# Optimization experiments

Measured on AMD Instinct MI355X. Metric: run time of the kernel, lower is better.

## Reference

```python
import jax, jax.numpy as jnp
import numpy as np
import math

N = 50000        # nodes
E = 800000       # edges
FEATS = 64
CLASSES = 16
HIDDEN = 64
DEPTH = 10
DIFF = 0.9
EMB_DIM = 1 + int(math.log2(FEATS))   # 7
ADJ_HID = 4 + EMB_DIM                  # 11


def setup_inputs() -> dict:
    key = jax.random.key(0)
    ks = jax.random.split(key, 12)
    x = jax.random.normal(ks[0], (N, FEATS), dtype=jnp.float32)
    src = jax.random.randint(ks[1], (E,), 0, N, dtype=jnp.int64)
    dst = jax.random.randint(ks[2], (E,), 0, N, dtype=jnp.int64)
    s = 0.05
    W1 = jax.random.normal(ks[3], (2 * FEATS, HIDDEN), jnp.float32) * s
    b1 = jnp.zeros((HIDDEN,), jnp.float32)
    W2 = jax.random.normal(ks[4], (HIDDEN, CLASSES), jnp.float32) * s
    b2 = jnp.zeros((CLASSES,), jnp.float32)
    A1 = jax.random.normal(ks[5], (2 + EMB_DIM, ADJ_HID), jnp.float32) * s
    ab1 = jnp.zeros((ADJ_HID,), jnp.float32)
    A2 = jax.random.normal(ks[6], (ADJ_HID, 1), jnp.float32) * s
    ab2 = jnp.zeros((1,), jnp.float32)
    emb = jax.random.normal(ks[7], (FEATS, EMB_DIM), jnp.float32) * s
    return {"x": x, "src": src, "dst": dst, "W1": W1, "b1": b1,
            "W2": W2, "b2": b2, "A1": A1, "ab1": ab1, "A2": A2,
            "ab2": ab2, "emb": emb}


def reference(x, src, dst, W1, b1, W2, b2, A1, ab1, A2, ab2, emb):
    n, f = x.shape
    # cached symmetric GCN normalization: D^-1/2 A D^-1/2
    deg = jax.ops.segment_sum(jnp.ones((src.shape[0],), x.dtype), dst, num_segments=n)
    inv_sqrt = jnp.where(deg > 0, jax.lax.rsqrt(jnp.maximum(deg, 1e-12)), 0.0)
    norm = inv_sqrt[src] * inv_sqrt[dst]   # [E]

    def conv(z):
        return jax.ops.segment_sum(z[src] * norm[:, None], dst, num_segments=n)

    # first diffusion loop (personalized-pagerank style residual blend)
    h0 = x
    z = x
    for _ in range(DEPTH):
        z = conv(z) * DIFF + (1.0 - DIFF) * h0

    # node x class pair MLP (class-major flatten, matching x.t().reshape(-1,1))
    cls = jnp.repeat(jnp.arange(f), n)                 # [f*n]
    pairs = jnp.concatenate([z.T.reshape(-1, 1),
                             h0.T.reshape(-1, 1),
                             emb[cls]], axis=1)        # [f*n, 2+EMB_DIM]
    u = jax.nn.relu(pairs @ A1 + ab1)
    u = (u @ A2 + ab2) / 2.0                           # [f*n, 1]
    z = u.reshape(f, n).T                              # [n, f]

    # dropout is identity in eval mode
    z = jnp.concatenate([z, h0], axis=1)               # [n, 2f]
    z = jax.nn.relu(z @ W1 + b1)
    z = z @ W2 + b2                                    # [n, classes]

    # second diffusion loop over class logits
    g0 = z
    for _ in range(DEPTH):
        z = conv(z) * DIFF + (1.0 - DIFF) * g0
    return z
```

## Files before the change

kernel.cpp:

```cpp
#include <hip/hip_runtime.h>

#define FEATS    64
#define CLASSES  16
#define EMB_DIM  7
#define ADJ_HID  11
#define DIFF     0.9f

__device__ inline float bf2f(unsigned short u) {
    return __uint_as_float(((unsigned int)u) << 16);
}
__device__ inline unsigned short f2bf(float f) {
    unsigned int u = __float_as_uint(f);
    return (unsigned short)((u + 0x7FFFu + ((u >> 16) & 1u)) >> 16);
}


__global__ __launch_bounds__(256) void k_deg(const int* __restrict__ dst, int* __restrict__ deg, int e) {
    int i = blockIdx.x * 256 + threadIdx.x;
    if (i < e) atomicAdd(&deg[dst[i]], 1);
}

__global__ __launch_bounds__(256) void k_invs(const int* __restrict__ deg, float* __restrict__ invs, int n) {
    int i = blockIdx.x * 256 + threadIdx.x;
    if (i < n) { int d = deg[i]; invs[i] = d > 0 ? rsqrtf((float)d) : 0.f; }
}

__global__ __launch_bounds__(256) void k_scan1(const int* __restrict__ deg, int* __restrict__ rowptr,
                                               int* __restrict__ bsum, int n) {
    __shared__ int s[256];
    int tid = threadIdx.x;
    int i = blockIdx.x * 256 + tid;
    int v = (i < n) ? deg[i] : 0;
    s[tid] = v; __syncthreads();
    for (int ofs = 1; ofs < 256; ofs <<= 1) {
        int t = (tid >= ofs) ? s[tid - ofs] : 0;
        __syncthreads(); s[tid] += t; __syncthreads();
    }
    if (i < n) rowptr[i] = s[tid] - v;
    if (tid == 255) bsum[blockIdx.x] = s[255];
}

__global__ __launch_bounds__(256) void k_scan2(int* __restrict__ bsum, int nb) {
    __shared__ int s[256];
    int tid = threadIdx.x;
    int v = (tid < nb) ? bsum[tid] : 0;
    s[tid] = v; __syncthreads();
    for (int ofs = 1; ofs < 256; ofs <<= 1) {
        int t = (tid >= ofs) ? s[tid - ofs] : 0;
        __syncthreads(); s[tid] += t; __syncthreads();
    }
    if (tid < nb) bsum[tid] = s[tid] - v;
}

__global__ __launch_bounds__(256) void k_scan3(int* __restrict__ rowptr, const int* __restrict__ bsum,
                                               int n, int e) {
    int i = blockIdx.x * 256 + threadIdx.x;
    if (i < n) rowptr[i] += bsum[i >> 8];
    if (i == n) rowptr[n] = e;
}

__global__ __launch_bounds__(256) void k_scatter(const int* __restrict__ src, const int* __restrict__ dst,
                                                 const float* __restrict__ invs, const int* __restrict__ rowptr,
                                                 int* __restrict__ cnt, int2* __restrict__ edge, int e) {
    int i = blockIdx.x * 256 + threadIdx.x;
    if (i >= e) return;
    int d = dst[i], sv = src[i];
    int pos = rowptr[d] + atomicAdd(&cnt[d], 1);
    edge[pos] = make_int2(sv, __float_as_int(invs[sv] * invs[d]));
}


__global__ __launch_bounds__(256) void k_cast(const float4* __restrict__ in, ushort4* __restrict__ out, int total4) {
    int i = blockIdx.x * 256 + threadIdx.x;
    if (i < total4) {
        float4 v = in[i];
        ushort4 o;
        o.x = f2bf(v.x); o.y = f2bf(v.y); o.z = f2bf(v.z); o.w = f2bf(v.w);
        out[i] = o;
    }
}


__global__ __launch_bounds__(256) void k_conv64b(const ushort4* __restrict__ zin, const ushort4* __restrict__ h0b,
                                                 ushort4* __restrict__ zout, const int* __restrict__ rowptr,
                                                 const int2* __restrict__ edge, int n) {
    int wid = (blockIdx.x * 256 + threadIdx.x) >> 6;
    if (wid >= n) return;
    int lane = threadIdx.x & 63;
    int g = lane >> 4, c = lane & 15;
    int e0 = rowptr[wid], e1 = rowptr[wid + 1];
    float a0 = 0.f, a1 = 0.f, a2 = 0.f, a3 = 0.f;
    for (int e = e0; e < e1; e += 16) {
        #pragma unroll
        for (int k = 0; k < 4; ++k) {
            int idx = e + k * 4 + g;
            bool ok = idx < e1;
            int2 p = edge[ok ? idx : e0];
            float w = ok ? __int_as_float(p.y) : 0.f;
            ushort4 v = zin[(size_t)p.x * 16 + c];
            a0 = fmaf(w, bf2f(v.x), a0);
            a1 = fmaf(w, bf2f(v.y), a1);
            a2 = fmaf(w, bf2f(v.z), a2);
            a3 = fmaf(w, bf2f(v.w), a3);
        }
    }
    a0 += __shfl_xor(a0, 16); a1 += __shfl_xor(a1, 16);
    a2 += __shfl_xor(a2, 16); a3 += __shfl_xor(a3, 16);
    a0 += __shfl_xor(a0, 32); a1 += __shfl_xor(a1, 32);
    a2 += __shfl_xor(a2, 32); a3 += __shfl_xor(a3, 32);
    if (lane < 16) {
        ushort4 h4 = h0b[(size_t)wid * 16 + lane];
        ushort4 o;
        o.x = f2bf(a0 * DIFF + (1.f - DIFF) * bf2f(h4.x));
        o.y = f2bf(a1 * DIFF + (1.f - DIFF) * bf2f(h4.y));
        o.z = f2bf(a2 * DIFF + (1.f - DIFF) * bf2f(h4.z));
        o.w = f2bf(a3 * DIFF + (1.f - DIFF) * bf2f(h4.w));
        zout[(size_t)wid * 16 + lane] = o;
    }
}


__global__ __launch_bounds__(256) void k_conv16(const float4* __restrict__ zin4, const float4* __restrict__ g04,
                                                float4* __restrict__ zout4, const int* __restrict__ rowptr,
                                                const int2* __restrict__ edge, int n) {
    int wid = (blockIdx.x * 256 + threadIdx.x) >> 6;
    if (wid >= n) return;
    int lane = threadIdx.x & 63;
    int g = lane >> 2, c = lane & 3;
    int e0 = rowptr[wid], e1 = rowptr[wid + 1];
    float4 acc; acc.x = acc.y = acc.z = acc.w = 0.f;
    for (int e = e0; e < e1; e += 32) {
        #pragma unroll
        for (int k = 0; k < 2; ++k) {
            int idx = e + k * 16 + g;
            bool ok = idx < e1;
            int2 p = edge[ok ? idx : e0];
            float w = ok ? __int_as_float(p.y) : 0.f;
            float4 v = zin4[(size_t)p.x * 4 + c];
            acc.x = fmaf(w, v.x, acc.x);
            acc.y = fmaf(w, v.y, acc.y);
            acc.z = fmaf(w, v.z, acc.z);
            acc.w = fmaf(w, v.w, acc.w);
        }
    }
    float4 t;
    t.x = __shfl_xor(acc.x, 4);  t.y = __shfl_xor(acc.y, 4);  t.z = __shfl_xor(acc.z, 4);  t.w = __shfl_xor(acc.w, 4);
    acc.x += t.x; acc.y += t.y; acc.z += t.z; acc.w += t.w;
    t.x = __shfl_xor(acc.x, 8);  t.y = __shfl_xor(acc.y, 8);  t.z = __shfl_xor(acc.z, 8);  t.w = __shfl_xor(acc.w, 8);
    acc.x += t.x; acc.y += t.y; acc.z += t.z; acc.w += t.w;
    t.x = __shfl_xor(acc.x, 16); t.y = __shfl_xor(acc.y, 16); t.z = __shfl_xor(acc.z, 16); t.w = __shfl_xor(acc.w, 16);
    acc.x += t.x; acc.y += t.y; acc.z += t.z; acc.w += t.w;
    t.x = __shfl_xor(acc.x, 32); t.y = __shfl_xor(acc.y, 32); t.z = __shfl_xor(acc.z, 32); t.w = __shfl_xor(acc.w, 32);
    acc.x += t.x; acc.y += t.y; acc.z += t.z; acc.w += t.w;
    if (lane < 4) {
        float4 h = g04[(size_t)wid * 4 + lane];
        float4 o;
        o.x = acc.x * DIFF + (1.f - DIFF) * h.x;
        o.y = acc.y * DIFF + (1.f - DIFF) * h.y;
        o.z = acc.z * DIFF + (1.f - DIFF) * h.z;
        o.w = acc.w * DIFF + (1.f - DIFF) * h.w;
        zout4[(size_t)wid * 4 + lane] = o;
    }
}


#define PM_GRID 512

__global__ __launch_bounds__(256) void k_pairmlp(const unsigned short* __restrict__ z1, const float* __restrict__ x,
                                                 const float* __restrict__ W1, const float* __restrict__ b1,
                                                 const float* __restrict__ W2, const float* __restrict__ b2,
                                                 const float* __restrict__ A1, const float* __restrict__ ab1,
                                                 const float* __restrict__ A2, const float* __restrict__ ab2,
                                                 const float* __restrict__ emb,
                                                 float* __restrict__ g0, int n, int ntiles) {
    __shared__ float W1s[128 * 64];
    __shared__ float W2s[64 * 16];
    __shared__ float in_s[32][128];
    __shared__ float hid[32 * 65];
    __shared__ float eA1T[ADJ_HID * 64];
    __shared__ float a0s[ADJ_HID], a1s[ADJ_HID], a2s[ADJ_HID];
    __shared__ float ab2s;

    int tid = threadIdx.x;
    const ushort4* z4p = (const ushort4*)z1;
    const float4*  x4p = (const float4*)x;

    #pragma unroll
    for (int k = 0; k < 32; ++k) W1s[tid + k * 256] = W1[tid + k * 256];
    #pragma unroll
    for (int k = 0; k < 4; ++k)  W2s[tid + k * 256] = W2[tid + k * 256];
    if (tid < ADJ_HID) { a0s[tid] = A1[tid]; a1s[tid] = A1[ADJ_HID + tid]; a2s[tid] = A2[tid]; }
    if (tid == 0) ab2s = ab2[0];
    for (int idx = tid; idx < ADJ_HID * 64; idx += 256) {
        int h = idx >> 6, c = idx & 63;
        float s = ab1[h];
        #pragma unroll
        for (int j = 0; j < EMB_DIM; j++) s = fmaf(emb[c * EMB_DIM + j], A1[(2 + j) * ADJ_HID + h], s);
        eA1T[idx] = s;
    }
    __syncthreads();

    for (int tile = blockIdx.x; tile < ntiles; tile += PM_GRID) {
        int base = tile * 32;

        #pragma unroll
        for (int j = 0; j < 2; ++j) {
            int e4 = tid + j * 256;
            int nl = e4 >> 4, c4 = e4 & 15;
            int node = base + nl; if (node > n - 1) node = n - 1;
            ushort4 z4 = z4p[(size_t)node * 16 + c4];
            float4  x4 = x4p[(size_t)node * 16 + c4];
            float zf0 = bf2f(z4.x), zf1 = bf2f(z4.y), zf2 = bf2f(z4.z), zf3 = bf2f(z4.w);
            float o0 = ab2s, o1 = ab2s, o2 = ab2s, o3 = ab2s;
            #pragma unroll
            for (int h = 0; h < ADJ_HID; h++) {
                float a0 = a0s[h], a1 = a1s[h], a2 = a2s[h];
                float4 ee = *(const float4*)&eA1T[h * 64 + c4 * 4];
                float t;
                t = fmaf(zf0, a0, fmaf(x4.x, a1, ee.x)); t = fmaxf(t, 0.f); o0 = fmaf(t, a2, o0);
                t = fmaf(zf1, a0, fmaf(x4.y, a1, ee.y)); t = fmaxf(t, 0.f); o1 = fmaf(t, a2, o1);
                t = fmaf(zf2, a0, fmaf(x4.z, a1, ee.z)); t = fmaxf(t, 0.f); o2 = fmaf(t, a2, o2);
                t = fmaf(zf3, a0, fmaf(x4.w, a1, ee.w)); t = fmaxf(t, 0.f); o3 = fmaf(t, a2, o3);
            }
            *(float4*)&in_s[nl][c4 * 4]      = make_float4(o0 * 0.5f, o1 * 0.5f, o2 * 0.5f, o3 * 0.5f);
            *(float4*)&in_s[nl][64 + c4 * 4] = x4;
        }
        __syncthreads();

        {
            int lane = tid & 63, wv = tid >> 6;
            int nb0 = wv * 8;
            float bv = b1[lane];
            float acc[8];
            #pragma unroll
            for (int j = 0; j < 8; ++j) acc[j] = bv;
            #pragma unroll 8
            for (int rb = 0; rb < 128; rb += 4) {
                float w0 = W1s[(rb    ) * 64 + lane];
                float w1 = W1s[(rb + 1) * 64 + lane];
                float w2 = W1s[(rb + 2) * 64 + lane];
                float w3 = W1s[(rb + 3) * 64 + lane];
                #pragma unroll
                for (int j = 0; j < 8; ++j) {
                    float4 iv = *(const float4*)&in_s[nb0 + j][rb];
                    acc[j] = fmaf(iv.w, w3, fmaf(iv.z, w2, fmaf(iv.y, w1, fmaf(iv.x, w0, acc[j]))));
                }
            }
            #pragma unroll
            for (int j = 0; j < 8; ++j) hid[(nb0 + j) * 65 + lane] = fmaxf(acc[j], 0.f);
        }
        __syncthreads();

        {
            int c  = tid & 15;
            int nl = tid >> 4;
            float ac0 = b2[c], ac1 = ac0;
            #pragma unroll
            for (int h = 0; h < 64; ++h) {
                float w = W2s[h * 16 + c];
                ac0 = fmaf(hid[nl * 65 + h],        w, ac0);
                ac1 = fmaf(hid[(nl + 16) * 65 + h], w, ac1);
            }
            int n0 = base + nl, n1 = base + nl + 16;
            if (n0 < n) g0[(size_t)n0 * 16 + c] = ac0;
            if (n1 < n) g0[(size_t)n1 * 16 + c] = ac1;
        }
        __syncthreads();
    }
}


extern "C" void kernel_launch(void* const* d_in, const int* in_sizes, int n_in,
                              void* d_out, int out_size, void* d_ws, size_t ws_size,
                              hipStream_t stream) {
    const float* x   = (const float*)d_in[0];
    const int*   src = (const int*)d_in[1];
    const int*   dst = (const int*)d_in[2];
    const float* W1  = (const float*)d_in[3];
    const float* b1  = (const float*)d_in[4];
    const float* W2  = (const float*)d_in[5];
    const float* b2  = (const float*)d_in[6];
    const float* A1  = (const float*)d_in[7];
    const float* ab1 = (const float*)d_in[8];
    const float* A2  = (const float*)d_in[9];
    const float* ab2 = (const float*)d_in[10];
    const float* emb = (const float*)d_in[11];

    int n = in_sizes[0] / FEATS;
    int e = in_sizes[1];

    char* ws = (char*)d_ws;
    size_t off = 0;
    auto alloc = [&](size_t bytes) {
        void* p = ws + off;
        off += bytes;
        off = (off + 255) & ~(size_t)255;
        return p;
    };

    int*     deg    = (int*)    alloc((size_t)n * 4);
    float*   invs   = (float*)  alloc((size_t)n * 4);
    int*     rowptr = (int*)    alloc((size_t)(n + 1) * 4);
    int*     cnt    = (int*)    alloc((size_t)n * 4);
    int*     bsum   = (int*)    alloc(1024);
    int2*    edge   = (int2*)   alloc((size_t)e * 8 + 256);
    ushort4* xb     = (ushort4*)alloc((size_t)n * 64 * 2);
    ushort4* zbA    = (ushort4*)alloc((size_t)n * 64 * 2);
    ushort4* zbB    = (ushort4*)alloc((size_t)n * 64 * 2);
    float*   g0     = (float*)  alloc((size_t)n * 16 * 4);
    float*   g1     = (float*)  alloc((size_t)n * 16 * 4);
    float*   g2     = (float*)  alloc((size_t)n * 16 * 4);

    hipMemsetAsync(deg, 0, (size_t)n * 4, stream);
    hipMemsetAsync(cnt, 0, (size_t)n * 4, stream);

    int eb = (e + 255) / 256;
    int nb = (n + 255) / 256;

    k_deg    <<<eb, 256, 0, stream>>>(dst, deg, e);
    k_invs   <<<nb, 256, 0, stream>>>(deg, invs, n);
    k_scan1  <<<nb, 256, 0, stream>>>(deg, rowptr, bsum, n);
    k_scan2  <<<1, 256, 0, stream>>>(bsum, nb);
    k_scan3  <<<(n + 256) / 256, 256, 0, stream>>>(rowptr, bsum, n, e);
    k_scatter<<<eb, 256, 0, stream>>>(src, dst, invs, rowptr, cnt, edge, e);

    int total4 = n * 16;
    k_cast<<<(total4 + 255) / 256, 256, 0, stream>>>((const float4*)x, xb, total4);

    int nwb = (n + 3) / 4;

    const ushort4* zin = xb;
    ushort4* zout = zbA;
    for (int it = 0; it < 10; ++it) {
        k_conv64b<<<nwb, 256, 0, stream>>>(zin, xb, zout, rowptr, edge, n);
        zin  = zout;
        zout = (it == 0) ? zbB : ((zout == zbA) ? zbB : zbA);
    }
    const unsigned short* z1 = (const unsigned short*)zin;

    int ntiles = (n + 31) / 32;
    k_pairmlp<<<PM_GRID, 256, 0, stream>>>(z1, x, W1, b1, W2, b2,
                                           A1, ab1, A2, ab2, emb, g0, n, ntiles);

    const float* gin = g0;
    float* gout = g1;
    for (int it = 0; it < 10; ++it) {
        float* out = (it == 9) ? (float*)d_out : gout;
        k_conv16<<<nwb, 256, 0, stream>>>((const float4*)gin, (const float4*)g0, (float4*)out,
                                          rowptr, edge, n);
        gin  = out;
        gout = (gout == g1) ? g2 : g1;
    }
}
```

Before: 683.3 us.

## Batch edge loads in 64-wide conv, shrink pair-MLP tiles and widen grid

The 64-feature bf16 conv kernel now takes a fast path for nodes with at most 16 edges. For higher-degree nodes it preloads the first 32 edge records into registers before issuing the gathers, so more memory requests are in flight at once. The pair-MLP kernel halves its tile to 16 nodes and raises its grid from 512 to 768 blocks, cutting shared memory per block and spreading tiles over more blocks. The 16-class conv reduction is also rewritten as an equivalent loop. The costs are more registers in the conv kernel and more W1 shared-memory loads per node in the MLP.

```diff
diff --git a/kernel.cpp b/kernel.cpp
--- a/kernel.cpp
+++ b/kernel.cpp
@@ -90,10 +90,11 @@
     int g = lane >> 4, c = lane & 15;
     int e0 = rowptr[wid], e1 = rowptr[wid + 1];
     float a0 = 0.f, a1 = 0.f, a2 = 0.f, a3 = 0.f;
-    for (int e = e0; e < e1; e += 16) {
+
+    if (e1 - e0 <= 16) {
         #pragma unroll
         for (int k = 0; k < 4; ++k) {
-            int idx = e + k * 4 + g;
+            int idx = e0 + k * 4 + g;
             bool ok = idx < e1;
             int2 p = edge[ok ? idx : e0];
             float w = ok ? __int_as_float(p.y) : 0.f;
@@ -103,7 +104,39 @@
             a2 = fmaf(w, bf2f(v.z), a2);
             a3 = fmaf(w, bf2f(v.w), a3);
         }
-    }
+    } else {
+        int2 P[8];
+        #pragma unroll
+        for (int k = 0; k < 8; ++k) {
+            int idx = e0 + k * 4 + g;
+            P[k] = edge[idx < e1 ? idx : e0];
+        }
+        #pragma unroll
+        for (int k = 0; k < 8; ++k) {
+            int idx = e0 + k * 4 + g;
+            float w = (idx < e1) ? __int_as_float(P[k].y) : 0.f;
+            ushort4 v = zin[(size_t)P[k].x * 16 + c];
+            a0 = fmaf(w, bf2f(v.x), a0);
+            a1 = fmaf(w, bf2f(v.y), a1);
+            a2 = fmaf(w, bf2f(v.z), a2);
+            a3 = fmaf(w, bf2f(v.w), a3);
+        }
+        for (int e = e0 + 32; e < e1; e += 16) {
+            #pragma unroll
+            for (int k = 0; k < 4; ++k) {
+                int idx = e + k * 4 + g;
+                bool ok = idx < e1;
+                int2 p = edge[ok ? idx : e0];
+                float w = ok ? __int_as_float(p.y) : 0.f;
+                ushort4 v = zin[(size_t)p.x * 16 + c];
+                a0 = fmaf(w, bf2f(v.x), a0);
+                a1 = fmaf(w, bf2f(v.y), a1);
+                a2 = fmaf(w, bf2f(v.z), a2);
+                a3 = fmaf(w, bf2f(v.w), a3);
+            }
+        }
+    }
+
     a0 += __shfl_xor(a0, 16); a1 += __shfl_xor(a1, 16);
     a2 += __shfl_xor(a2, 16); a3 += __shfl_xor(a3, 16);
     a0 += __shfl_xor(a0, 32); a1 += __shfl_xor(a1, 32);
@@ -143,15 +176,13 @@
             acc.w = fmaf(w, v.w, acc.w);
         }
     }
-    float4 t;
-    t.x = __shfl_xor(acc.x, 4);  t.y = __shfl_xor(acc.y, 4);  t.z = __shfl_xor(acc.z, 4);  t.w = __shfl_xor(acc.w, 4);
-    acc.x += t.x; acc.y += t.y; acc.z += t.z; acc.w += t.w;
-    t.x = __shfl_xor(acc.x, 8);  t.y = __shfl_xor(acc.y, 8);  t.z = __shfl_xor(acc.z, 8);  t.w = __shfl_xor(acc.w, 8);
-    acc.x += t.x; acc.y += t.y; acc.z += t.z; acc.w += t.w;
-    t.x = __shfl_xor(acc.x, 16); t.y = __shfl_xor(acc.y, 16); t.z = __shfl_xor(acc.z, 16); t.w = __shfl_xor(acc.w, 16);
-    acc.x += t.x; acc.y += t.y; acc.z += t.z; acc.w += t.w;
-    t.x = __shfl_xor(acc.x, 32); t.y = __shfl_xor(acc.y, 32); t.z = __shfl_xor(acc.z, 32); t.w = __shfl_xor(acc.w, 32);
-    acc.x += t.x; acc.y += t.y; acc.z += t.z; acc.w += t.w;
+    #pragma unroll
+    for (int m = 4; m <= 32; m <<= 1) {
+        acc.x += __shfl_xor(acc.x, m);
+        acc.y += __shfl_xor(acc.y, m);
+        acc.z += __shfl_xor(acc.z, m);
+        acc.w += __shfl_xor(acc.w, m);
+    }
     if (lane < 4) {
         float4 h = g04[(size_t)wid * 4 + lane];
         float4 o;
@@ -164,7 +195,7 @@
 }
 
 
-#define PM_GRID 512
+#define PM_GRID 768
 
 __global__ __launch_bounds__(256) void k_pairmlp(const unsigned short* __restrict__ z1, const float* __restrict__ x,
                                                  const float* __restrict__ W1, const float* __restrict__ b1,
@@ -175,8 +206,8 @@
                                                  float* __restrict__ g0, int n, int ntiles) {
     __shared__ float W1s[128 * 64];
     __shared__ float W2s[64 * 16];
-    __shared__ float in_s[32][128];
-    __shared__ float hid[32 * 65];
+    __shared__ float in_s[16][128];
+    __shared__ float hid[16 * 65];
     __shared__ float eA1T[ADJ_HID * 64];
     __shared__ float a0s[ADJ_HID], a1s[ADJ_HID], a2s[ADJ_HID];
     __shared__ float ab2s;
@@ -201,12 +232,10 @@
     __syncthreads();
 
     for (int tile = blockIdx.x; tile < ntiles; tile += PM_GRID) {
-        int base = tile * 32;
-
-        #pragma unroll
-        for (int j = 0; j < 2; ++j) {
-            int e4 = tid + j * 256;
-            int nl = e4 >> 4, c4 = e4 & 15;
+        int base = tile * 16;
+
+        {
+            int nl = tid >> 4, c4 = tid & 15;
             int node = base + nl; if (node > n - 1) node = n - 1;
             ushort4 z4 = z4p[(size_t)node * 16 + c4];
             float4  x4 = x4p[(size_t)node * 16 + c4];
@@ -229,11 +258,11 @@
 
         {
             int lane = tid & 63, wv = tid >> 6;
-            int nb0 = wv * 8;
+            int nb0 = wv * 4;
             float bv = b1[lane];
-            float acc[8];
-            #pragma unroll
-            for (int j = 0; j < 8; ++j) acc[j] = bv;
+            float acc[4];
+            #pragma unroll
+            for (int j = 0; j < 4; ++j) acc[j] = bv;
             #pragma unroll 8
             for (int rb = 0; rb < 128; rb += 4) {
                 float w0 = W1s[(rb    ) * 64 + lane];
@@ -241,29 +270,25 @@
                 float w2 = W1s[(rb + 2) * 64 + lane];
                 float w3 = W1s[(rb + 3) * 64 + lane];
                 #pragma unroll
-                for (int j = 0; j < 8; ++j) {
+                for (int j = 0; j < 4; ++j) {
                     float4 iv = *(const float4*)&in_s[nb0 + j][rb];
                     acc[j] = fmaf(iv.w, w3, fmaf(iv.z, w2, fmaf(iv.y, w1, fmaf(iv.x, w0, acc[j]))));
                 }
             }
             #pragma unroll
-            for (int j = 0; j < 8; ++j) hid[(nb0 + j) * 65 + lane] = fmaxf(acc[j], 0.f);
+            for (int j = 0; j < 4; ++j) hid[(nb0 + j) * 65 + lane] = fmaxf(acc[j], 0.f);
         }
         __syncthreads();
 
         {
             int c  = tid & 15;
             int nl = tid >> 4;
-            float ac0 = b2[c], ac1 = ac0;
-            #pragma unroll
-            for (int h = 0; h < 64; ++h) {
-                float w = W2s[h * 16 + c];
-                ac0 = fmaf(hid[nl * 65 + h],        w, ac0);
-                ac1 = fmaf(hid[(nl + 16) * 65 + h], w, ac1);
-            }
-            int n0 = base + nl, n1 = base + nl + 16;
-            if (n0 < n) g0[(size_t)n0 * 16 + c] = ac0;
-            if (n1 < n) g0[(size_t)n1 * 16 + c] = ac1;
+            float ac = b2[c];
+            #pragma unroll
+            for (int h = 0; h < 64; ++h)
+                ac = fmaf(hid[nl * 65 + h], W2s[h * 16 + c], ac);
+            int n0 = base + nl;
+            if (n0 < n) g0[(size_t)n0 * 16 + c] = ac;
         }
         __syncthreads();
     }
@@ -338,7 +363,7 @@
     }
     const unsigned short* z1 = (const unsigned short*)zin;
 
-    int ntiles = (n + 31) / 32;
+    int ntiles = (n + 15) / 16;
     k_pairmlp<<<PM_GRID, 256, 0, stream>>>(z1, x, W1, b1, W2, b2,
                                            A1, ab1, A2, ab2, emb, g0, n, ntiles);
 
```

Result: faster. 628.9 us (-8.0%).
